# Kernel tuning notes

Hardware: AMD Instinct MI355X
Metric: run time of the kernel (lower is better)

## Reference

```python
import jax, jax.numpy as jnp
import numpy as np
from jax import lax

PATCH = 15
WIDTH_DCP = 55


def _box_sum(x, r):
    # AvgPool2d(kernel=2r+1, stride=1, padding=r, count_include_pad=True) * (2r+1)^2;
    # the kernel-size factor cancels in all mean_*/N ratios below.
    return lax.reduce_window(x, 0.0, lax.add, (1, 1, 2 * r + 1, 2 * r + 1),
                             (1, 1, 1, 1), ((0, 0), (0, 0), (r, r), (r, r)))


def _guided_filter(I, p, r, eps):
    Nn = _box_sum(jnp.ones_like(p), r)
    mean_I = _box_sum(I, r) / Nn
    mean_p = _box_sum(p, r) / Nn
    mean_Ip = _box_sum(I * p, r) / Nn
    cov_Ip = mean_Ip - mean_I * mean_p
    mean_II = _box_sum(I * I, r) / Nn
    var_I = mean_II - mean_I * mean_I
    a = cov_Ip / (var_I + eps)
    b = mean_p - a * mean_I
    mean_a = _box_sum(a, r) / Nn
    mean_b = _box_sum(b, r) / Nn
    return mean_a * I + mean_b


def _dark_channel(x):
    d = x.min(axis=1, keepdims=True)
    pad = WIDTH_DCP // 2
    d = jnp.pad(d, ((0, 0), (0, 0), (pad, pad), (pad, pad)), constant_values=1.0)
    return lax.reduce_window(d, jnp.inf, lax.min, (1, 1, WIDTH_DCP, WIDTH_DCP),
                             (1, 1, 1, 1), 'VALID')


def _map_A(x):
    N, C, H, W = x.shape
    dc = _dark_channel(x).reshape(N, -1)
    k = int(H * W * 0.001)
    _, idx = lax.top_k(dc, k)  # brightest dark-channel pixels
    xr = x.reshape(N, 3, -1)
    searched = jnp.take_along_axis(xr, jnp.broadcast_to(idx[:, None, :], (N, 3, k)), axis=2)
    A = searched.mean(axis=2)
    return jnp.broadcast_to(A[:, :, None, None], x.shape)


def _t_bccr(haze, mapA, ps):
    t1 = (mapA - haze) / (mapA - 20.0 / 255.0)
    t2 = (mapA - haze) / (mapA - 300.0 / 255.0)
    t = jnp.maximum(t1, t2).max(axis=1, keepdims=True)
    pad = ps // 2
    t = jnp.pad(t, ((0, 0), (0, 0), (pad, pad), (pad, pad)), constant_values=0.0)
    t = lax.reduce_window(t, -jnp.inf, lax.max, (1, 1, ps, ps), (1, 1, 1, 1), 'VALID')
    return jnp.clip(t, 0.05, 1.0)


def _pad_reshape(data, ps):
    N, C, H, W = data.shape
    pad_H = (ps - H % ps) % ps
    pad_W = (ps - W % ps) % ps
    padded = jnp.pad(data, ((0, 0), (0, 0), (pad_H // 2, pad_H - pad_H // 2),
                            (pad_W // 2, pad_W - pad_W // 2)), mode='edge')
    nH = padded.shape[2] // ps
    nW = padded.shape[3] // ps
    p = padded[:, 0].reshape(N, nH, ps, nW, ps).transpose(0, 1, 3, 2, 4)
    p = p.reshape(N, nH * nW, ps * ps).transpose(0, 2, 1)  # [N, ps*ps, P]
    return p, pad_H // 2, pad_W // 2, nH, nW


def _transmission(S, V1, ps, pixel_number=10, slp_length=0.1):
    X, sH, sW, nH, nW = _pad_reshape(V1, ps)  # [N, pp, P]
    Y, _, _, _, _ = _pad_reshape(S, ps)
    dX = X[:, :, None, :] - X[:, None, :, :]          # [N, pp, pp, P]
    dY = Y[:, :, None, :] - Y[:, None, :, :]
    slope = dY / (dX + 1e-8)
    smask = ((slope > -1) & (slope < 0)).astype(X.dtype)
    scount = smask.sum(axis=2)                         # [N, pp, P]
    pmask = (scount >= 0.5 * ps * ps).astype(X.dtype)
    pcount = pmask.sum(axis=1, keepdims=True)          # [N, 1, P]
    mx = (X * pmask).sum(axis=1, keepdims=True) / (pcount + 1e-5)
    my = (Y * pmask).sum(axis=1, keepdims=True) / (pcount + 1e-5)
    k = ((X * Y * pmask).sum(axis=1, keepdims=True) - pcount * mx * my) / (
        ((X * pmask) ** 2).sum(axis=1, keepdims=True) - pcount * mx ** 2 + 1e-5)
    b = my - k * mx
    t = 1.0 + k / (b + 1e-8)
    length = (1.0 + k ** 2) ** 0.5 * ((X * pmask).max(axis=1, keepdims=True)
                                      - (X + 1e8 * (1.0 - pmask)).min(axis=1, keepdims=True))
    tmask = ((pcount > pixel_number) & (length > slp_length) & (k > -1) & (k < 0)
             & (t > 0.01) & (t < 1 - 0.01)).astype(X.dtype)
    t = (t * tmask).reshape(-1, 1, nH, nW)
    t = jnp.repeat(jnp.repeat(t, ps, axis=2), ps, axis=3)  # nearest upsample x ps
    return t[:, :, sH:S.shape[2] + sH, sW:S.shape[3] + sW]


def _percentile(t, bili=0.05):
    N = t.shape[0]
    flat = jnp.where(t > 0, t, 10.0).reshape(N, -1)
    s = jnp.sort(flat, axis=1)
    n = flat.shape[1]
    idx = min(int(bili * n), n - 1)
    return s[:, idx].reshape(-1, 1, 1, 1)


def _restore(image, ps=PATCH):
    mapA = _map_A(image)
    norm = image / mapA
    mx = norm.max(axis=1, keepdims=True)
    S = 1.0 - norm.min(axis=1, keepdims=True) / (mx + 1e-8)
    V1 = 1.0 / (mx + 1e-8)
    t1 = _transmission(S, V1, ps)
    half = ps // 2
    t2 = _transmission(S[:, :, half:, half:], V1[:, :, half:, half:], ps)
    t2 = jnp.pad(t2, ((0, 0), (0, 0), (half, 0), (half, 0)), constant_values=0.0)
    t_slp = jnp.where((t1 != 0) & (t2 != 0), (t1 + t2) / 2.0,
                      jnp.where(t1 != 0, t1, t2))
    t_bl = _t_bccr(image, mapA, ps)
    t_min = _percentile(t_slp)
    t_fusion = jnp.clip(jnp.where(t_slp > 0, t_slp, t_bl), t_min, 1.0)
    t_ref = _guided_filter(image.mean(axis=1, keepdims=True), t_fusion, 2 * ps, 1e-3)
    return (image - mapA) / t_ref + mapA


def setup_inputs() -> dict:
    key = jax.random.key(0)
    image = jax.random.uniform(key, (1, 3, 480, 480), dtype=jnp.float32)
    return {"image": image}


def reference(image):
    return _restore(image)
```

## Files before the change

### kernel.cpp

```cpp
#include <hip/hip_runtime.h>
#include <math.h>

#define W 480
#define HT 480
#define HW (W*HT)
#define GE (HW/256)
#define PP 225
#define NPATCH 1024
#define EQCAP 8192

struct State {
  unsigned histA[4][256];
  unsigned slotP[4];
  unsigned slotK[4];
  float sumA[3];
  unsigned eqCount;
  float A[3];
  unsigned tminbits;
  unsigned eqIdx[EQCAP];
  float tp1[NPATCH];
  float tp2[NPATCH];
};

__device__ __forceinline__ void resolve_level(const unsigned* __restrict__ h,
                                              unsigned k_in, int desc,
                                              unsigned* lds,
                                              unsigned& chosen, unsigned& k_out) {
  int t = threadIdx.x;
  unsigned c = h[desc ? (255 - t) : t];
  lds[t] = c;
  __syncthreads();
  for (int s = 1; s < 256; s <<= 1) {
    unsigned add = (t >= s) ? lds[t - s] : 0u;
    __syncthreads();
    lds[t] += add;
    __syncthreads();
  }
  unsigned incl = lds[t];
  unsigned excl = incl - c;
  if (incl >= k_in && excl < k_in) { lds[256] = (unsigned)t; lds[257] = k_in - excl; }
  __syncthreads();
  unsigned tt = lds[256];
  k_out = lds[257];
  chosen = desc ? (255u - tt) : tt;
  __syncthreads();
}

__global__ __launch_bounds__(512) void k_rowmin(const float* __restrict__ img,
                                                float* __restrict__ rowmin, State* st) {
  __shared__ float l[534];
  int y = blockIdx.x, t = threadIdx.x;
  for (int i = t; i < 534; i += 512) {
    int col = i - 27;
    float v = 1.0f;
    if ((unsigned)col < (unsigned)W) {
      int q = y * W + col;
      v = fminf(fminf(img[q], img[HW + q]), img[2 * HW + q]);
    }
    l[i] = v;
  }
  if (y == 0 && t < 256) {
    for (int i = 0; i < 4; ++i) st->histA[i][t] = 0u;
    if (t == 0) { st->sumA[0] = 0.f; st->sumA[1] = 0.f; st->sumA[2] = 0.f; st->eqCount = 0u; }
  }
  __syncthreads();
  if (t < W) {
    float m = l[t];
    for (int d = 1; d < 55; ++d) m = fminf(m, l[t + d]);
    rowmin[y * W + t] = m;
  }
}

__global__ __launch_bounds__(256) void k_vchunk(const float* __restrict__ rowmin,
                                                float* __restrict__ cmin) {
  int p = blockIdx.x * 256 + threadIdx.x;
  if (p >= 60 * W) return;
  int c = p / W, x = p - c * W;
  float m = INFINITY;
  for (int r = 0; r < 8; ++r) m = fminf(m, rowmin[(c * 8 + r) * W + x]);
  cmin[p] = m;
}

__global__ __launch_bounds__(256) void k_minV2(const float* __restrict__ rowmin,
                                               const float* __restrict__ cmin,
                                               float* __restrict__ dc, State* st) {
  __shared__ unsigned lh[256];
  int t = threadIdx.x;
  lh[t] = 0u;
  __syncthreads();
  int p = blockIdx.x * 256 + t;
  int y = p / W, x = p - y * W;
  int lo = y - 27, hi = y + 27;
  float m = (lo < 0 || hi >= HT) ? 1.0f : INFINITY;
  int lo2 = max(lo, 0), hi2 = min(hi, HT - 1);
  int cs = (lo2 + 7) >> 3, ce = ((hi2 + 1) >> 3) - 1;
  for (int c = cs; c <= ce; ++c) m = fminf(m, cmin[c * W + x]);
  for (int yy = lo2; yy < (cs << 3); ++yy) m = fminf(m, rowmin[yy * W + x]);
  for (int yy = (ce + 1) << 3; yy <= hi2; ++yy) m = fminf(m, rowmin[yy * W + x]);
  dc[p] = m;
  atomicAdd(&lh[__float_as_uint(m) >> 24], 1u);
  __syncthreads();
  unsigned c = lh[t];
  if (c) atomicAdd(&st->histA[0][t], c);
}

__global__ __launch_bounds__(256) void k_hist(const float* __restrict__ dc,
                                              State* st, int level) {
  __shared__ unsigned lds[258];
  int t = threadIdx.x;
  unsigned prefix, k;
  if (level == 1) { prefix = 0u; k = 230u; }
  else { prefix = st->slotP[level - 2]; k = st->slotK[level - 2]; }
  unsigned ch, kn;
  resolve_level(st->histA[level - 1], k, 1, lds, ch, kn);
  prefix |= ch << (32 - 8 * level);
  k = kn;
  if (t == 0) { st->slotP[level - 1] = prefix; st->slotK[level - 1] = k; }
  __syncthreads();
  lds[t] = 0u;
  __syncthreads();
  int p = blockIdx.x * 256 + t;
  unsigned bits = __float_as_uint(dc[p]);
  unsigned mask = 0xFFFFFFFFu << (32 - 8 * level);
  if ((bits & mask) == prefix)
    atomicAdd(&lds[(bits >> (24 - 8 * level)) & 0xFFu], 1u);
  __syncthreads();
  unsigned c = lds[t];
  if (c) atomicAdd(&st->histA[level][t], c);
}

__global__ __launch_bounds__(256) void k_gatherA(const float* __restrict__ dc,
                                                 const float* __restrict__ img, State* st) {
  __shared__ unsigned lds[258];
  int t = threadIdx.x;
  unsigned prefix = st->slotP[2], k = st->slotK[2];
  unsigned ch, kn;
  resolve_level(st->histA[3], k, 1, lds, ch, kn);
  unsigned vb = prefix | ch;
  if (t == 0) { st->slotP[3] = vb; st->slotK[3] = kn; }
  int p = blockIdx.x * 256 + t;
  unsigned bits = __float_as_uint(dc[p]);
  if (bits > vb) {
    atomicAdd(&st->sumA[0], img[p]);
    atomicAdd(&st->sumA[1], img[HW + p]);
    atomicAdd(&st->sumA[2], img[2 * HW + p]);
  } else if (bits == vb) {
    unsigned pos = atomicAdd(&st->eqCount, 1u);
    if (pos < (unsigned)EQCAP) st->eqIdx[pos] = (unsigned)p;
  }
}

__global__ __launch_bounds__(256) void k_finalizeA(const float* __restrict__ img, State* st) {
  __shared__ unsigned lds[258];
  __shared__ unsigned lh[256];
  __shared__ unsigned sIdx[EQCAP];
  __shared__ float ssum[3];
  int t = threadIdx.x;
  unsigned keq = st->slotK[3];
  unsigned ne = st->eqCount; if (ne > (unsigned)EQCAP) ne = EQCAP;
  for (int i = t; i < (int)ne; i += 256) sIdx[i] = st->eqIdx[i];
  if (t < 3) ssum[t] = 0.f;
  __syncthreads();
  unsigned pfx = 0u, k = keq;
  for (int lev = 0; lev < 3; ++lev) {
    int s = 16 - 8 * lev;
    lh[t] = 0u;
    __syncthreads();
    for (int i = t; i < (int)ne; i += 256) {
      unsigned v = sIdx[i];
      if ((v >> (s + 8)) == (pfx >> (s + 8)))
        atomicAdd(&lh[(v >> s) & 0xFFu], 1u);
    }
    __syncthreads();
    unsigned ch, kn;
    resolve_level(lh, k, 0, lds, ch, kn);
    pfx |= ch << s;
    k = kn;
  }
  float a0 = 0.f, a1 = 0.f, a2 = 0.f;
  for (int i = t; i < (int)ne; i += 256) {
    unsigned q = sIdx[i];
    if (q <= pfx) { a0 += img[q]; a1 += img[HW + q]; a2 += img[2 * HW + q]; }
  }
  atomicAdd(&ssum[0], a0); atomicAdd(&ssum[1], a1); atomicAdd(&ssum[2], a2);
  __syncthreads();
  if (t == 0) {
    st->A[0] = (st->sumA[0] + ssum[0]) / 230.0f;
    st->A[1] = (st->sumA[1] + ssum[1]) / 230.0f;
    st->A[2] = (st->sumA[2] + ssum[2]) / 230.0f;
  }
}

__global__ __launch_bounds__(256) void k_elem1(const float* __restrict__ img,
                                               const State* __restrict__ st,
                                               float2* __restrict__ SV,
                                               float* __restrict__ Io, float* __restrict__ To) {
  int p = blockIdx.x * 256 + threadIdx.x;
  float A0 = st->A[0], A1 = st->A[1], A2 = st->A[2];
  float r = img[p], g = img[HW + p], bl = img[2 * HW + p];
  float nr = r / A0, ng = g / A1, nb = bl / A2;
  float mx = fmaxf(fmaxf(nr, ng), nb);
  float mn = fminf(fminf(nr, ng), nb);
  float d = mx + 1e-8f;
  float S = 1.0f - mn / d;
  float V = 1.0f / d;
  SV[p] = make_float2(V, S);
  Io[p] = ((r + g) + bl) / 3.0f;
  const float c20 = (float)(20.0 / 255.0);
  const float c300 = (float)(300.0 / 255.0);
  float t0 = fmaxf((A0 - r) / (A0 - c20), (A0 - r) / (A0 - c300));
  float t1 = fmaxf((A1 - g) / (A1 - c20), (A1 - g) / (A1 - c300));
  float t2 = fmaxf((A2 - bl) / (A2 - c20), (A2 - bl) / (A2 - c300));
  To[p] = fmaxf(fmaxf(t0, t1), t2);
}

__device__ __forceinline__ float wred_sum(float v) { for (int m = 32; m; m >>= 1) v += __shfl_xor(v, m, 64); return v; }
__device__ __forceinline__ float wred_max(float v) { for (int m = 32; m; m >>= 1) v = fmaxf(v, __shfl_xor(v, m, 64)); return v; }
__device__ __forceinline__ float wred_min(float v) { for (int m = 32; m; m >>= 1) v = fminf(v, __shfl_xor(v, m, 64)); return v; }

__global__ __launch_bounds__(256) void k_mega1(const float2* __restrict__ SV,
                                               const float* __restrict__ To,
                                               float* __restrict__ mh, State* st) {
  __shared__ float2 XY[PP];
  __shared__ float part[4][8];
  int b = blockIdx.x;
  int t = threadIdx.x;
  if (b >= 2048) {
    int p = (b - 2048) * 256 + t;
    int y = p / W, x = p - y * W;
    float m = -INFINITY;
    for (int d = -7; d <= 7; ++d) {
      int xx = x + d;
      float v = ((unsigned)xx < (unsigned)W) ? To[y * W + xx] : 0.0f;
      m = fmaxf(m, v);
    }
    mh[p] = m;
    return;
  }
  int mode = b >> 10;
  int pid = b & 1023;
  int ph = pid >> 5, pw = pid & 31;
  if (t < PP) {
    int r = t / 15, c = t - (t / 15) * 15;
    int y, x;
    if (mode == 0) { y = ph * 15 + r; x = pw * 15 + c; }
    else {
      y = ph * 15 + r + 4; y = (y < 7) ? 7 : ((y > 479) ? 479 : y);
      x = pw * 15 + c + 4; x = (x < 7) ? 7 : ((x > 479) ? 479 : x);
    }
    XY[t] = SV[y * W + x];
  }
  __syncthreads();
  float xi = 0.f, yi = 0.f;
  int cnt = 0;
  if (t < PP) {
    xi = XY[t].x; yi = XY[t].y;
    for (int j = 0; j < PP; ++j) {
      float2 o = XY[j];
      float dY = yi - o.y;
      float D = (xi - o.x) + 1e-8f;
      cnt += ((dY * D < 0.0f) && (fabsf(dY) < fabsf(D))) ? 1 : 0;
    }
  }
  float pmf = (t < PP && cnt >= 113) ? 1.0f : 0.0f;
  float xm = xi * pmf, ym = yi * pmf;
  float v0 = wred_sum(pmf);
  float v1 = wred_sum(xm);
  float v2 = wred_sum(ym);
  float v3 = wred_sum(xm * ym);
  float v4 = wred_sum(xm * xm);
  float v5 = wred_max((t < PP) ? xm : -INFINITY);
  float v6 = wred_min((t < PP) ? (xi + 1e8f * (1.0f - pmf)) : INFINITY);
  int wid = t >> 6, lane = t & 63;
  if (lane == 0) {
    part[wid][0] = v0; part[wid][1] = v1; part[wid][2] = v2; part[wid][3] = v3;
    part[wid][4] = v4; part[wid][5] = v5; part[wid][6] = v6;
  }
  __syncthreads();
  if (t == 0) {
    float pcount = 0.f, sx = 0.f, sy = 0.f, sxy = 0.f, sxx = 0.f;
    float mxX = -INFINITY, mnX = INFINITY;
    for (int w2 = 0; w2 < 4; ++w2) {
      pcount += part[w2][0]; sx += part[w2][1]; sy += part[w2][2];
      sxy += part[w2][3]; sxx += part[w2][4];
      mxX = fmaxf(mxX, part[w2][5]); mnX = fminf(mnX, part[w2][6]);
    }
    float den = pcount + 1e-5f;
    float mxv = sx / den, myv = sy / den;
    float kk = (sxy - pcount * mxv * myv) / (sxx - pcount * (mxv * mxv) + 1e-5f);
    float bb = myv - kk * mxv;
    float tt = 1.0f + kk / (bb + 1e-8f);
    float len = sqrtf(1.0f + kk * kk) * (mxX - mnX);
    bool m = (pcount > 10.0f) && (len > 0.1f) && (kk > -1.0f) && (kk < 0.0f)
             && (tt > 0.01f) && (tt < 0.99f);
    float res = tt * (m ? 1.0f : 0.0f);
    if (mode == 0) st->tp1[pid] = res; else st->tp2[pid] = res;
  }
}

__global__ __launch_bounds__(256) void k_maxV_pct(const float* __restrict__ mh,
                                                  float* __restrict__ tb, State* st) {
  __shared__ unsigned lh[256];
  __shared__ unsigned lds[258];
  __shared__ float tp1s[NPATCH], tp2s[NPATCH];
  int b = blockIdx.x;
  int t = threadIdx.x;
  if (b < GE) {
    int p = b * 256 + t;
    int y = p / W, x = p - y * W;
    float m = -INFINITY;
    for (int d = -7; d <= 7; ++d) {
      int yy = y + d;
      float v = ((unsigned)yy < (unsigned)HT) ? mh[yy * W + x] : 0.0f;
      m = fmaxf(m, v);
    }
    tb[p] = fminf(fmaxf(m, 0.05f), 1.0f);
    return;
  }
  for (int i = t; i < NPATCH; i += 256) { tp1s[i] = st->tp1[i]; tp2s[i] = st->tp2[i]; }
  __syncthreads();
  unsigned prefix = 0u, k = 11521u;
  for (int level = 0; level < 4; ++level) {
    lh[t] = 0u;
    __syncthreads();
    unsigned mask = (level == 0) ? 0u : (0xFFFFFFFFu << (32 - 8 * level));
    int shift = 24 - 8 * level;
    for (int i = t; i < NPATCH; i += 256) {
      int ph = i >> 5, pw = i & 31;
      float a = tp1s[i];
      int rcnt[2], ridx[2], ccnt[2], cidx[2];
      if (ph == 0) { rcnt[0] = 7; ridx[0] = -1; rcnt[1] = 8; ridx[1] = 0; }
      else         { rcnt[0] = 4; ridx[0] = ph - 1; rcnt[1] = 11; ridx[1] = ph; }
      if (pw == 0) { ccnt[0] = 7; cidx[0] = -1; ccnt[1] = 8; cidx[1] = 0; }
      else         { ccnt[0] = 4; cidx[0] = pw - 1; ccnt[1] = 11; cidx[1] = pw; }
      for (int ri = 0; ri < 2; ++ri)
        for (int ci = 0; ci < 2; ++ci) {
          unsigned area = (unsigned)(rcnt[ri] * ccnt[ci]);
          float bb = 0.0f;
          if (ridx[ri] >= 0 && cidx[ci] >= 0) bb = tp2s[ridx[ri] * 32 + cidx[ci]];
          float r;
          if (a != 0.0f && bb != 0.0f) r = (a + bb) / 2.0f;
          else r = (a != 0.0f) ? a : bb;
          float u = (r > 0.0f) ? r : 10.0f;
          unsigned bits = __float_as_uint(u);
          if ((bits & mask) == prefix)
            atomicAdd(&lh[(bits >> shift) & 0xFFu], area);
        }
    }
    __syncthreads();
    unsigned ch, kn;
    resolve_level(lh, k, 0, lds, ch, kn);
    prefix |= ch << shift;
    k = kn;
  }
  if (t == 0) st->tminbits = prefix;
}

__global__ __launch_bounds__(512) void k_gf1h(const float* __restrict__ I,
                                              const float* __restrict__ tb,
                                              const State* __restrict__ st,
                                              float4* __restrict__ box4) {
  __shared__ float tp1s[NPATCH], tp2s[NPATCH];
  __shared__ float Pl[540], Il[540];
  int y = blockIdx.x, t = threadIdx.x;
  for (int i = t; i < NPATCH; i += 512) { tp1s[i] = st->tp1[i]; tp2s[i] = st->tp2[i]; }
  __syncthreads();
  float tmin = __uint_as_float(st->tminbits);
  int c1row = (y / 15) * 32;
  bool c2ok = (y >= 7);
  int c2row = c2ok ? ((y - 4) / 15) * 32 : 0;
  for (int i = t; i < 540; i += 512) {
    int col = i - 30;
    float pv = 0.0f, iv = 0.0f;
    if ((unsigned)col < (unsigned)W) {
      int q = y * W + col;
      float a = tp1s[c1row + col / 15];
      float bb = 0.0f;
      if (c2ok && col >= 7) bb = tp2s[c2row + (col - 4) / 15];
      float r;
      if (a != 0.0f && bb != 0.0f) r = (a + bb) / 2.0f;
      else r = (a != 0.0f) ? a : bb;
      float v = (r > 0.0f) ? r : tb[q];
      v = (v < tmin) ? tmin : v;
      v = (v > 1.0f) ? 1.0f : v;
      pv = v; iv = I[q];
    }
    Pl[i] = pv; Il[i] = iv;
  }
  __syncthreads();
  if (t < W) {
    float sI = 0.f, sP = 0.f, sIp = 0.f, sII = 0.f;
    for (int d = 0; d < 61; ++d) {
      float iv = Il[t + d], pv = Pl[t + d];
      sI += iv; sP += pv; sIp += iv * pv; sII += iv * iv;
    }
    box4[y * W + t] = make_float4(sI, sP, sIp, sII);
  }
}

__global__ __launch_bounds__(256) void k_gf1v(const float4* __restrict__ box4,
                                              float2* __restrict__ ab) {
  int p = blockIdx.x * 256 + threadIdx.x;
  int y = p / W, x = p - y * W;
  float sI = 0.f, sP = 0.f, sIp = 0.f, sII = 0.f;
  for (int d = -30; d <= 30; ++d) {
    int yy = y + d;
    if ((unsigned)yy < (unsigned)HT) {
      float4 v = box4[yy * W + x];
      sI += v.x; sP += v.y; sIp += v.z; sII += v.w;
    }
  }
  int ny = min(y + 30, HT - 1) - max(y - 30, 0) + 1;
  int nx = min(x + 30, W - 1) - max(x - 30, 0) + 1;
  float Nn = (float)(ny * nx);
  float mI = sI / Nn, mP = sP / Nn, mIp = sIp / Nn, mII = sII / Nn;
  float cov = mIp - mI * mP;
  float var = mII - mI * mI;
  float av = cov / (var + 1e-3f);
  ab[p] = make_float2(av, mP - av * mI);
}

__global__ __launch_bounds__(512) void k_gf2h(const float2* __restrict__ ab,
                                              float2* __restrict__ hab) {
  __shared__ float2 l[540];
  int y = blockIdx.x, t = threadIdx.x;
  for (int i = t; i < 540; i += 512) {
    int col = i - 30;
    float2 v = make_float2(0.f, 0.f);
    if ((unsigned)col < (unsigned)W) v = ab[y * W + col];
    l[i] = v;
  }
  __syncthreads();
  if (t < W) {
    float sa = 0.f, sb = 0.f;
    for (int d = 0; d < 61; ++d) { float2 v = l[t + d]; sa += v.x; sb += v.y; }
    hab[y * W + t] = make_float2(sa, sb);
  }
}

__global__ __launch_bounds__(256) void k_gf2vfin(const float2* __restrict__ hab,
                                                 const float* __restrict__ I,
                                                 const float* __restrict__ img,
                                                 const State* __restrict__ st,
                                                 float* __restrict__ out) {
  int p = blockIdx.x * 256 + threadIdx.x;
  int y = p / W, x = p - y * W;
  float sa = 0.f, sb = 0.f;
  for (int d = -30; d <= 30; ++d) {
    int yy = y + d;
    if ((unsigned)yy < (unsigned)HT) { float2 v = hab[yy * W + x]; sa += v.x; sb += v.y; }
  }
  int ny = min(y + 30, HT - 1) - max(y - 30, 0) + 1;
  int nx = min(x + 30, W - 1) - max(x - 30, 0) + 1;
  float Nn = (float)(ny * nx);
  float tref = (sa / Nn) * I[p] + (sb / Nn);
  float A0 = st->A[0], A1 = st->A[1], A2 = st->A[2];
  out[p]          = (img[p]          - A0) / tref + A0;
  out[HW + p]     = (img[HW + p]     - A1) / tref + A1;
  out[2 * HW + p] = (img[2 * HW + p] - A2) / tref + A2;
}

extern "C" void kernel_launch(void* const* d_in, const int* in_sizes, int n_in,
                              void* d_out, int out_size, void* d_ws, size_t ws_size,
                              hipStream_t stream) {
  (void)in_sizes; (void)n_in; (void)out_size; (void)ws_size;
  const float* img = (const float*)d_in[0];
  float* out = (float*)d_out;
  State* st = (State*)d_ws;
  float* sb = (float*)((char*)d_ws + 65536);
  float* bufA = sb;
  float* bufB = sb + HW;
  float* bufD = sb + 2 * HW;
  float* bufF = sb + 3 * HW;
  float2* SV   = (float2*)bufF;
  float* cmin  = bufF + 2 * HW;
  float* mh    = bufF + 3 * HW;
  float4* box4 = (float4*)bufF;
  float2* hab  = (float2*)bufF;
  float2* ab   = (float2*)(sb + 7 * HW);

  dim3 b256(256), b512(512);
  dim3 ge(GE), rows(HT);

  k_rowmin<<<rows, b512, 0, stream>>>(img, bufB, st);
  k_vchunk<<<dim3(113), b256, 0, stream>>>(bufB, cmin);
  k_minV2<<<ge, b256, 0, stream>>>(bufB, cmin, bufA, st);
  for (int l = 1; l < 4; ++l)
    k_hist<<<ge, b256, 0, stream>>>(bufA, st, l);
  k_gatherA<<<ge, b256, 0, stream>>>(bufA, img, st);
  k_finalizeA<<<dim3(1), b256, 0, stream>>>(img, st);
  k_elem1<<<ge, b256, 0, stream>>>(img, st, SV, bufD, bufB);
  k_mega1<<<dim3(2048 + GE), b256, 0, stream>>>(SV, bufB, mh, st);
  k_maxV_pct<<<dim3(GE + 1), b256, 0, stream>>>(mh, bufA, st);
  k_gf1h<<<rows, b512, 0, stream>>>(bufD, bufA, st, box4);
  k_gf1v<<<ge, b256, 0, stream>>>(box4, ab);
  k_gf2h<<<rows, b512, 0, stream>>>(ab, hab);
  k_gf2vfin<<<ge, b256, 0, stream>>>(hab, bufD, img, st, out);
}
```

Measured before the change: 192.7 us.

## Fuse radix-select levels via last-block tickets and process two rows per thread

Each histogram pass now resolves its own radix digit in the last block to finish, using an atomic ticket. This removes the separate resolve step and one full histogram pass, and the final byte plus the tie-break are handled in a fused gather kernel. The bccr max filter's horizontal pass is fused into a row-wise elementwise kernel that uses shared memory. The vertical box and max filters process two rows per thread with a sliding update, halving their grids. These changes cut kernel launches and redundant memory reads, but add a serial tail in the last block and rely on memory fences for correctness.

New measurement: 283.7 us. 47.2% more time.

```diff
diff --git a/kernel.cpp b/kernel.cpp
--- a/kernel.cpp
+++ b/kernel.cpp
@@ -4,15 +4,15 @@
 #define W 480
 #define HT 480
 #define HW (W*HT)
-#define GE (HW/256)
+#define GE 900
 #define PP 225
 #define NPATCH 1024
 #define EQCAP 8192
 
 struct State {
-  unsigned histA[4][256];
-  unsigned slotP[4];
-  unsigned slotK[4];
+  unsigned histA[3][256];
+  unsigned slotP[3], slotK[3];
+  unsigned tickets[8];
   float sumA[3];
   unsigned eqCount;
   float A[3];
@@ -22,12 +22,29 @@
   float tp2[NPATCH];
 };
 
+__device__ __forceinline__ unsigned aload(const unsigned* p) {
+  return __hip_atomic_load(p, __ATOMIC_RELAXED, __HIP_MEMORY_SCOPE_AGENT);
+}
+
+__device__ __forceinline__ bool last_block(unsigned* ticket, unsigned nb) {
+  __shared__ unsigned isl;
+  __syncthreads();
+  if (threadIdx.x == 0) {
+    __threadfence();
+    unsigned tk = __hip_atomic_fetch_add(ticket, 1u, __ATOMIC_ACQ_REL, __HIP_MEMORY_SCOPE_AGENT);
+    isl = (tk == nb - 1u) ? 1u : 0u;
+  }
+  __syncthreads();
+  return isl != 0u;
+}
+
 __device__ __forceinline__ void resolve_level(const unsigned* __restrict__ h,
-                                              unsigned k_in, int desc,
+                                              unsigned k_in, int desc, int glob,
                                               unsigned* lds,
                                               unsigned& chosen, unsigned& k_out) {
   int t = threadIdx.x;
-  unsigned c = h[desc ? (255 - t) : t];
+  int idx = desc ? (255 - t) : t;
+  unsigned c = glob ? aload(&h[idx]) : h[idx];
   lds[t] = c;
   __syncthreads();
   for (int s = 1; s < 256; s <<= 1) {
@@ -60,7 +77,8 @@
     l[i] = v;
   }
   if (y == 0 && t < 256) {
-    for (int i = 0; i < 4; ++i) st->histA[i][t] = 0u;
+    for (int i = 0; i < 3; ++i) st->histA[i][t] = 0u;
+    if (t < 8) st->tickets[t] = 0u;
     if (t == 0) { st->sumA[0] = 0.f; st->sumA[1] = 0.f; st->sumA[2] = 0.f; st->eqCount = 0u; }
   }
   __syncthreads();
@@ -85,6 +103,7 @@
                                                const float* __restrict__ cmin,
                                                float* __restrict__ dc, State* st) {
   __shared__ unsigned lh[256];
+  __shared__ unsigned lds[258];
   int t = threadIdx.x;
   lh[t] = 0u;
   __syncthreads();
@@ -102,141 +121,155 @@
   __syncthreads();
   unsigned c = lh[t];
   if (c) atomicAdd(&st->histA[0][t], c);
-}
-
-__global__ __launch_bounds__(256) void k_hist(const float* __restrict__ dc,
-                                              State* st, int level) {
+  if (last_block(&st->tickets[0], GE)) {
+    unsigned ch, kn;
+    resolve_level(st->histA[0], 230u, 1, 1, lds, ch, kn);
+    if (t == 0) { st->slotP[0] = ch << 24; st->slotK[0] = kn; }
+  }
+}
+
+__global__ __launch_bounds__(256) void k_histL(const float* __restrict__ dc,
+                                               State* st, int level) {
+  __shared__ unsigned lh[256];
   __shared__ unsigned lds[258];
   int t = threadIdx.x;
-  unsigned prefix, k;
-  if (level == 1) { prefix = 0u; k = 230u; }
-  else { prefix = st->slotP[level - 2]; k = st->slotK[level - 2]; }
-  unsigned ch, kn;
-  resolve_level(st->histA[level - 1], k, 1, lds, ch, kn);
-  prefix |= ch << (32 - 8 * level);
-  k = kn;
-  if (t == 0) { st->slotP[level - 1] = prefix; st->slotK[level - 1] = k; }
-  __syncthreads();
-  lds[t] = 0u;
+  unsigned prefix = st->slotP[level - 1];
+  unsigned k = st->slotK[level - 1];
+  lh[t] = 0u;
   __syncthreads();
   int p = blockIdx.x * 256 + t;
   unsigned bits = __float_as_uint(dc[p]);
   unsigned mask = 0xFFFFFFFFu << (32 - 8 * level);
   if ((bits & mask) == prefix)
-    atomicAdd(&lds[(bits >> (24 - 8 * level)) & 0xFFu], 1u);
-  __syncthreads();
-  unsigned c = lds[t];
+    atomicAdd(&lh[(bits >> (24 - 8 * level)) & 0xFFu], 1u);
+  __syncthreads();
+  unsigned c = lh[t];
   if (c) atomicAdd(&st->histA[level][t], c);
-}
-
-__global__ __launch_bounds__(256) void k_gatherA(const float* __restrict__ dc,
-                                                 const float* __restrict__ img, State* st) {
+  if (last_block(&st->tickets[level], GE)) {
+    unsigned ch, kn;
+    resolve_level(st->histA[level], k, 1, 1, lds, ch, kn);
+    if (t == 0) { st->slotP[level] = prefix | (ch << (24 - 8 * level)); st->slotK[level] = kn; }
+  }
+}
+
+__global__ __launch_bounds__(256) void k_gather24(const float* __restrict__ dc,
+                                                  const float* __restrict__ img, State* st) {
+  __shared__ unsigned sPk[EQCAP];
+  __shared__ unsigned lh[256];
   __shared__ unsigned lds[258];
+  __shared__ float ssum[3];
   int t = threadIdx.x;
-  unsigned prefix = st->slotP[2], k = st->slotK[2];
-  unsigned ch, kn;
-  resolve_level(st->histA[3], k, 1, lds, ch, kn);
-  unsigned vb = prefix | ch;
-  if (t == 0) { st->slotP[3] = vb; st->slotK[3] = kn; }
+  unsigned pfx24 = st->slotP[2];
+  unsigned k24 = st->slotK[2];
   int p = blockIdx.x * 256 + t;
   unsigned bits = __float_as_uint(dc[p]);
-  if (bits > vb) {
+  unsigned top24 = bits & 0xFFFFFF00u;
+  if (top24 > pfx24) {
     atomicAdd(&st->sumA[0], img[p]);
     atomicAdd(&st->sumA[1], img[HW + p]);
     atomicAdd(&st->sumA[2], img[2 * HW + p]);
-  } else if (bits == vb) {
+  } else if (top24 == pfx24) {
     unsigned pos = atomicAdd(&st->eqCount, 1u);
-    if (pos < (unsigned)EQCAP) st->eqIdx[pos] = (unsigned)p;
-  }
-}
-
-__global__ __launch_bounds__(256) void k_finalizeA(const float* __restrict__ img, State* st) {
-  __shared__ unsigned lds[258];
-  __shared__ unsigned lh[256];
-  __shared__ unsigned sIdx[EQCAP];
-  __shared__ float ssum[3];
-  int t = threadIdx.x;
-  unsigned keq = st->slotK[3];
-  unsigned ne = st->eqCount; if (ne > (unsigned)EQCAP) ne = EQCAP;
-  for (int i = t; i < (int)ne; i += 256) sIdx[i] = st->eqIdx[i];
-  if (t < 3) ssum[t] = 0.f;
-  __syncthreads();
-  unsigned pfx = 0u, k = keq;
-  for (int lev = 0; lev < 3; ++lev) {
-    int s = 16 - 8 * lev;
+    if (pos < (unsigned)EQCAP) st->eqIdx[pos] = ((bits & 0xFFu) << 24) | (unsigned)p;
+  }
+  if (last_block(&st->tickets[3], GE)) {
+    unsigned ne = st->eqCount; if (ne > (unsigned)EQCAP) ne = EQCAP;
+    for (int i = t; i < (int)ne; i += 256) sPk[i] = st->eqIdx[i];
+    if (t < 3) ssum[t] = 0.f;
     lh[t] = 0u;
     __syncthreads();
+    for (int i = t; i < (int)ne; i += 256) atomicAdd(&lh[sPk[i] >> 24], 1u);
+    __syncthreads();
+    unsigned lb, keq;
+    resolve_level(lh, k24, 1, 0, lds, lb, keq);
+    float a0 = 0.f, a1 = 0.f, a2 = 0.f;
     for (int i = t; i < (int)ne; i += 256) {
-      unsigned v = sIdx[i];
-      if ((v >> (s + 8)) == (pfx >> (s + 8)))
-        atomicAdd(&lh[(v >> s) & 0xFFu], 1u);
-    }
-    __syncthreads();
-    unsigned ch, kn;
-    resolve_level(lh, k, 0, lds, ch, kn);
-    pfx |= ch << s;
-    k = kn;
-  }
-  float a0 = 0.f, a1 = 0.f, a2 = 0.f;
-  for (int i = t; i < (int)ne; i += 256) {
-    unsigned q = sIdx[i];
-    if (q <= pfx) { a0 += img[q]; a1 += img[HW + q]; a2 += img[2 * HW + q]; }
-  }
-  atomicAdd(&ssum[0], a0); atomicAdd(&ssum[1], a1); atomicAdd(&ssum[2], a2);
-  __syncthreads();
-  if (t == 0) {
-    st->A[0] = (st->sumA[0] + ssum[0]) / 230.0f;
-    st->A[1] = (st->sumA[1] + ssum[1]) / 230.0f;
-    st->A[2] = (st->sumA[2] + ssum[2]) / 230.0f;
-  }
-}
-
-__global__ __launch_bounds__(256) void k_elem1(const float* __restrict__ img,
-                                               const State* __restrict__ st,
-                                               float2* __restrict__ SV,
-                                               float* __restrict__ Io, float* __restrict__ To) {
-  int p = blockIdx.x * 256 + threadIdx.x;
-  float A0 = st->A[0], A1 = st->A[1], A2 = st->A[2];
-  float r = img[p], g = img[HW + p], bl = img[2 * HW + p];
-  float nr = r / A0, ng = g / A1, nb = bl / A2;
-  float mx = fmaxf(fmaxf(nr, ng), nb);
-  float mn = fminf(fminf(nr, ng), nb);
-  float d = mx + 1e-8f;
-  float S = 1.0f - mn / d;
-  float V = 1.0f / d;
-  SV[p] = make_float2(V, S);
-  Io[p] = ((r + g) + bl) / 3.0f;
-  const float c20 = (float)(20.0 / 255.0);
-  const float c300 = (float)(300.0 / 255.0);
-  float t0 = fmaxf((A0 - r) / (A0 - c20), (A0 - r) / (A0 - c300));
-  float t1 = fmaxf((A1 - g) / (A1 - c20), (A1 - g) / (A1 - c300));
-  float t2 = fmaxf((A2 - bl) / (A2 - c20), (A2 - bl) / (A2 - c300));
-  To[p] = fmaxf(fmaxf(t0, t1), t2);
+      unsigned v = sPk[i];
+      if ((v >> 24) > lb) {
+        unsigned q = v & 0x3FFFFu;
+        a0 += img[q]; a1 += img[HW + q]; a2 += img[2 * HW + q];
+      }
+    }
+    unsigned pfi = 0u, kk = keq;
+    for (int lev = 0; lev < 3; ++lev) {
+      int s = 16 - 8 * lev;
+      __syncthreads();
+      lh[t] = 0u;
+      __syncthreads();
+      for (int i = t; i < (int)ne; i += 256) {
+        unsigned v = sPk[i];
+        if ((v >> 24) == lb) {
+          unsigned idx = v & 0x3FFFFu;
+          if ((idx >> (s + 8)) == (pfi >> (s + 8)))
+            atomicAdd(&lh[(idx >> s) & 0xFFu], 1u);
+        }
+      }
+      __syncthreads();
+      unsigned ch, kn;
+      resolve_level(lh, kk, 0, 0, lds, ch, kn);
+      pfi |= ch << s;
+      kk = kn;
+    }
+    for (int i = t; i < (int)ne; i += 256) {
+      unsigned v = sPk[i];
+      if ((v >> 24) == lb) {
+        unsigned q = v & 0x3FFFFu;
+        if (q <= pfi) { a0 += img[q]; a1 += img[HW + q]; a2 += img[2 * HW + q]; }
+      }
+    }
+    atomicAdd(&ssum[0], a0); atomicAdd(&ssum[1], a1); atomicAdd(&ssum[2], a2);
+    __syncthreads();
+    if (t == 0) {
+      st->A[0] = (st->sumA[0] + ssum[0]) / 230.0f;
+      st->A[1] = (st->sumA[1] + ssum[1]) / 230.0f;
+      st->A[2] = (st->sumA[2] + ssum[2]) / 230.0f;
+    }
+  }
+}
+
+__global__ __launch_bounds__(512) void k_elem_row(const float* __restrict__ img,
+                                                  const State* __restrict__ st,
+                                                  float2* __restrict__ SV,
+                                                  float* __restrict__ Io,
+                                                  float* __restrict__ mh) {
+  __shared__ float Tl[494];
+  int y = blockIdx.x, t = threadIdx.x;
+  if (t < 7) Tl[t] = 0.0f;
+  if (t >= 480 && t < 487) Tl[t + 7] = 0.0f;
+  if (t < W) {
+    int p = y * W + t;
+    float A0 = st->A[0], A1 = st->A[1], A2 = st->A[2];
+    float r = img[p], g = img[HW + p], bl = img[2 * HW + p];
+    float nr = r / A0, ng = g / A1, nb = bl / A2;
+    float mx = fmaxf(fmaxf(nr, ng), nb);
+    float mn = fminf(fminf(nr, ng), nb);
+    float d = mx + 1e-8f;
+    SV[p] = make_float2(1.0f / d, 1.0f - mn / d);
+    Io[p] = ((r + g) + bl) / 3.0f;
+    const float c20 = (float)(20.0 / 255.0);
+    const float c300 = (float)(300.0 / 255.0);
+    float t0 = fmaxf((A0 - r) / (A0 - c20), (A0 - r) / (A0 - c300));
+    float t1 = fmaxf((A1 - g) / (A1 - c20), (A1 - g) / (A1 - c300));
+    float t2 = fmaxf((A2 - bl) / (A2 - c20), (A2 - bl) / (A2 - c300));
+    Tl[7 + t] = fmaxf(fmaxf(t0, t1), t2);
+  }
+  __syncthreads();
+  if (t < W) {
+    float m = Tl[t];
+    for (int d = 1; d < 15; ++d) m = fmaxf(m, Tl[t + d]);
+    mh[y * W + t] = m;
+  }
 }
 
 __device__ __forceinline__ float wred_sum(float v) { for (int m = 32; m; m >>= 1) v += __shfl_xor(v, m, 64); return v; }
 __device__ __forceinline__ float wred_max(float v) { for (int m = 32; m; m >>= 1) v = fmaxf(v, __shfl_xor(v, m, 64)); return v; }
 __device__ __forceinline__ float wred_min(float v) { for (int m = 32; m; m >>= 1) v = fminf(v, __shfl_xor(v, m, 64)); return v; }
 
-__global__ __launch_bounds__(256) void k_mega1(const float2* __restrict__ SV,
-                                               const float* __restrict__ To,
-                                               float* __restrict__ mh, State* st) {
+__global__ __launch_bounds__(256) void k_mega1(const float2* __restrict__ SV, State* st) {
   __shared__ float2 XY[PP];
   __shared__ float part[4][8];
   int b = blockIdx.x;
   int t = threadIdx.x;
-  if (b >= 2048) {
-    int p = (b - 2048) * 256 + t;
-    int y = p / W, x = p - y * W;
-    float m = -INFINITY;
-    for (int d = -7; d <= 7; ++d) {
-      int xx = x + d;
-      float v = ((unsigned)xx < (unsigned)W) ? To[y * W + xx] : 0.0f;
-      m = fmaxf(m, v);
-    }
-    mh[p] = m;
-    return;
-  }
   int mode = b >> 10;
   int pid = b & 1023;
   int ph = pid >> 5, pw = pid & 31;
@@ -305,16 +338,19 @@
   __shared__ float tp1s[NPATCH], tp2s[NPATCH];
   int b = blockIdx.x;
   int t = threadIdx.x;
-  if (b < GE) {
+  if (b < 450) {
     int p = b * 256 + t;
-    int y = p / W, x = p - y * W;
-    float m = -INFINITY;
-    for (int d = -7; d <= 7; ++d) {
-      int yy = y + d;
+    int x = p % W, yp = p / W;
+    int y0 = 2 * yp;
+    float m0 = -INFINITY, m1 = -INFINITY;
+    for (int d = 0; d < 16; ++d) {
+      int yy = y0 - 7 + d;
       float v = ((unsigned)yy < (unsigned)HT) ? mh[yy * W + x] : 0.0f;
-      m = fmaxf(m, v);
-    }
-    tb[p] = fminf(fmaxf(m, 0.05f), 1.0f);
+      if (d < 15) m0 = fmaxf(m0, v);
+      if (d > 0)  m1 = fmaxf(m1, v);
+    }
+    tb[y0 * W + x]       = fminf(fmaxf(m0, 0.05f), 1.0f);
+    tb[(y0 + 1) * W + x] = fminf(fmaxf(m1, 0.05f), 1.0f);
     return;
   }
   for (int i = t; i < NPATCH; i += 256) { tp1s[i] = st->tp1[i]; tp2s[i] = st->tp2[i]; }
@@ -349,7 +385,7 @@
     }
     __syncthreads();
     unsigned ch, kn;
-    resolve_level(lh, k, 0, lds, ch, kn);
+    resolve_level(lh, k, 0, 0, lds, ch, kn);
     prefix |= ch << shift;
     k = kn;
   }
@@ -401,23 +437,35 @@
 __global__ __launch_bounds__(256) void k_gf1v(const float4* __restrict__ box4,
                                               float2* __restrict__ ab) {
   int p = blockIdx.x * 256 + threadIdx.x;
-  int y = p / W, x = p - y * W;
+  int x = p % W, yp = p / W;
+  int y0 = 2 * yp, y1 = y0 + 1;
   float sI = 0.f, sP = 0.f, sIp = 0.f, sII = 0.f;
-  for (int d = -30; d <= 30; ++d) {
-    int yy = y + d;
-    if ((unsigned)yy < (unsigned)HT) {
-      float4 v = box4[yy * W + x];
-      sI += v.x; sP += v.y; sIp += v.z; sII += v.w;
-    }
-  }
-  int ny = min(y + 30, HT - 1) - max(y - 30, 0) + 1;
+  int lo = max(y0 - 30, 0), hi = min(y0 + 30, HT - 1);
+  for (int yy = lo; yy <= hi; ++yy) {
+    float4 v = box4[yy * W + x];
+    sI += v.x; sP += v.y; sIp += v.z; sII += v.w;
+  }
   int nx = min(x + 30, W - 1) - max(x - 30, 0) + 1;
-  float Nn = (float)(ny * nx);
-  float mI = sI / Nn, mP = sP / Nn, mIp = sIp / Nn, mII = sII / Nn;
-  float cov = mIp - mI * mP;
-  float var = mII - mI * mI;
-  float av = cov / (var + 1e-3f);
-  ab[p] = make_float2(av, mP - av * mI);
+  {
+    float Nn = (float)((hi - lo + 1) * nx);
+    float mI = sI / Nn, mP = sP / Nn, mIp = sIp / Nn, mII = sII / Nn;
+    float cov = mIp - mI * mP;
+    float var = mII - mI * mI;
+    float av = cov / (var + 1e-3f);
+    ab[y0 * W + x] = make_float2(av, mP - av * mI);
+  }
+  {
+    int yr = y0 - 30, ya = y0 + 31;
+    if (yr >= 0)  { float4 v = box4[yr * W + x]; sI -= v.x; sP -= v.y; sIp -= v.z; sII -= v.w; }
+    if (ya < HT)  { float4 v = box4[ya * W + x]; sI += v.x; sP += v.y; sIp += v.z; sII += v.w; }
+    int lo1 = max(y1 - 30, 0), hi1 = min(y1 + 30, HT - 1);
+    float Nn = (float)((hi1 - lo1 + 1) * nx);
+    float mI = sI / Nn, mP = sP / Nn, mIp = sIp / Nn, mII = sII / Nn;
+    float cov = mIp - mI * mP;
+    float var = mII - mI * mI;
+    float av = cov / (var + 1e-3f);
+    ab[y1 * W + x] = make_float2(av, mP - av * mI);
+  }
 }
 
 __global__ __launch_bounds__(512) void k_gf2h(const float2* __restrict__ ab,
@@ -444,20 +492,33 @@
                                                  const State* __restrict__ st,
                                                  float* __restrict__ out) {
   int p = blockIdx.x * 256 + threadIdx.x;
-  int y = p / W, x = p - y * W;
+  int x = p % W, yp = p / W;
+  int y0 = 2 * yp, y1 = y0 + 1;
+  float A0 = st->A[0], A1 = st->A[1], A2 = st->A[2];
   float sa = 0.f, sb = 0.f;
-  for (int d = -30; d <= 30; ++d) {
-    int yy = y + d;
-    if ((unsigned)yy < (unsigned)HT) { float2 v = hab[yy * W + x]; sa += v.x; sb += v.y; }
-  }
-  int ny = min(y + 30, HT - 1) - max(y - 30, 0) + 1;
+  int lo = max(y0 - 30, 0), hi = min(y0 + 30, HT - 1);
+  for (int yy = lo; yy <= hi; ++yy) { float2 v = hab[yy * W + x]; sa += v.x; sb += v.y; }
   int nx = min(x + 30, W - 1) - max(x - 30, 0) + 1;
-  float Nn = (float)(ny * nx);
-  float tref = (sa / Nn) * I[p] + (sb / Nn);
-  float A0 = st->A[0], A1 = st->A[1], A2 = st->A[2];
-  out[p]          = (img[p]          - A0) / tref + A0;
-  out[HW + p]     = (img[HW + p]     - A1) / tref + A1;
-  out[2 * HW + p] = (img[2 * HW + p] - A2) / tref + A2;
+  {
+    float Nn = (float)((hi - lo + 1) * nx);
+    int q = y0 * W + x;
+    float tref = (sa / Nn) * I[q] + (sb / Nn);
+    out[q]          = (img[q]          - A0) / tref + A0;
+    out[HW + q]     = (img[HW + q]     - A1) / tref + A1;
+    out[2 * HW + q] = (img[2 * HW + q] - A2) / tref + A2;
+  }
+  {
+    int yr = y0 - 30, ya = y0 + 31;
+    if (yr >= 0) { float2 v = hab[yr * W + x]; sa -= v.x; sb -= v.y; }
+    if (ya < HT) { float2 v = hab[ya * W + x]; sa += v.x; sb += v.y; }
+    int lo1 = max(y1 - 30, 0), hi1 = min(y1 + 30, HT - 1);
+    float Nn = (float)((hi1 - lo1 + 1) * nx);
+    int q = y1 * W + x;
+    float tref = (sa / Nn) * I[q] + (sb / Nn);
+    out[q]          = (img[q]          - A0) / tref + A0;
+    out[HW + q]     = (img[HW + q]     - A1) / tref + A1;
+    out[2 * HW + q] = (img[2 * HW + q] - A2) / tref + A2;
+  }
 }
 
 extern "C" void kernel_launch(void* const* d_in, const int* in_sizes, int n_in,
@@ -468,32 +529,30 @@
   float* out = (float*)d_out;
   State* st = (State*)d_ws;
   float* sb = (float*)((char*)d_ws + 65536);
-  float* bufA = sb;
-  float* bufB = sb + HW;
-  float* bufD = sb + 2 * HW;
-  float* bufF = sb + 3 * HW;
-  float2* SV   = (float2*)bufF;
-  float* cmin  = bufF + 2 * HW;
-  float* mh    = bufF + 3 * HW;
-  float4* box4 = (float4*)bufF;
-  float2* hab  = (float2*)bufF;
+  float* bufA  = sb;
+  float* bufRM = sb + HW;
+  float* bufI  = sb + 2 * HW;
+  float2* SV   = (float2*)(sb + 3 * HW);
+  float* cmin  = sb + 5 * HW;
+  float* mh    = sb + 6 * HW;
+  float4* box4 = (float4*)(sb + 3 * HW);
   float2* ab   = (float2*)(sb + 7 * HW);
+  float2* hab  = (float2*)(sb + 3 * HW);
 
   dim3 b256(256), b512(512);
-  dim3 ge(GE), rows(HT);
-
-  k_rowmin<<<rows, b512, 0, stream>>>(img, bufB, st);
-  k_vchunk<<<dim3(113), b256, 0, stream>>>(bufB, cmin);
-  k_minV2<<<ge, b256, 0, stream>>>(bufB, cmin, bufA, st);
-  for (int l = 1; l < 4; ++l)
-    k_hist<<<ge, b256, 0, stream>>>(bufA, st, l);
-  k_gatherA<<<ge, b256, 0, stream>>>(bufA, img, st);
-  k_finalizeA<<<dim3(1), b256, 0, stream>>>(img, st);
-  k_elem1<<<ge, b256, 0, stream>>>(img, st, SV, bufD, bufB);
-  k_mega1<<<dim3(2048 + GE), b256, 0, stream>>>(SV, bufB, mh, st);
-  k_maxV_pct<<<dim3(GE + 1), b256, 0, stream>>>(mh, bufA, st);
-  k_gf1h<<<rows, b512, 0, stream>>>(bufD, bufA, st, box4);
-  k_gf1v<<<ge, b256, 0, stream>>>(box4, ab);
+  dim3 ge(GE), rows(HT), half(450);
+
+  k_rowmin<<<rows, b512, 0, stream>>>(img, bufRM, st);
+  k_vchunk<<<dim3(113), b256, 0, stream>>>(bufRM, cmin);
+  k_minV2<<<ge, b256, 0, stream>>>(bufRM, cmin, bufA, st);
+  k_histL<<<ge, b256, 0, stream>>>(bufA, st, 1);
+  k_histL<<<ge, b256, 0, stream>>>(bufA, st, 2);
+  k_gather24<<<ge, b256, 0, stream>>>(bufA, img, st);
+  k_elem_row<<<rows, b512, 0, stream>>>(img, st, SV, bufI, mh);
+  k_mega1<<<dim3(2048), b256, 0, stream>>>(SV, st);
+  k_maxV_pct<<<dim3(451), b256, 0, stream>>>(mh, bufA, st);
+  k_gf1h<<<rows, b512, 0, stream>>>(bufI, bufA, st, box4);
+  k_gf1v<<<half, b256, 0, stream>>>(box4, ab);
   k_gf2h<<<rows, b512, 0, stream>>>(ab, hab);
-  k_gf2vfin<<<ge, b256, 0, stream>>>(hab, bufD, img, st, out);
-}
+  k_gf2vfin<<<half, b256, 0, stream>>>(hab, bufI, img, st, out);
+}
```
